# Kernel tuning notes

Measured on AMD Instinct MI355X. Metric: run time of the kernel, lower is better.

## Reference

```python
import jax, jax.numpy as jnp
import numpy as np

B, S, D = 2, 2048, 2048
H, KVH, DH = 16, 4, 128
WIN = 128
THETA = 10000.0  # local rope (layer_idx=0 -> local/sliding path)


def setup_inputs() -> dict:
    key = jax.random.key(0)
    ks = jax.random.split(key, 5)
    return {
        "x": jax.random.normal(ks[0], (B, S, D), dtype=jnp.float32),
        "Wq": jax.random.normal(ks[1], (H * DH, D), dtype=jnp.float32) * 0.02,
        "Wk": jax.random.normal(ks[2], (KVH * DH, D), dtype=jnp.float32) * 0.02,
        "Wv": jax.random.normal(ks[3], (KVH * DH, D), dtype=jnp.float32) * 0.02,
        "Wo": jax.random.normal(ks[4], (D, H * DH), dtype=jnp.float32) * 0.02,
    }


def _rotate_half(t):
    half = t.shape[-1] // 2
    return jnp.concatenate([-t[..., half:], t[..., :half]], axis=-1)


def _rope_tables(seq_len, head_dim, theta, dtype):
    inv_freq = 1.0 / (theta ** (jnp.arange(0, head_dim, 2, dtype=jnp.float32) / head_dim))
    freqs = jnp.arange(seq_len, dtype=jnp.float32)[:, None] * inv_freq[None, :]  # [S, DH/2]
    # source does repeat_interleave(cos, 2, dim=-1): [S, DH]
    cos = jnp.repeat(jnp.cos(freqs), 2, axis=-1).astype(dtype)
    sin = jnp.repeat(jnp.sin(freqs), 2, axis=-1).astype(dtype)
    return cos[None, :, None, :], sin[None, :, None, :]  # broadcast over [B,S,H,DH]


def reference(x, Wq, Wk, Wv, Wo):
    b, s, _ = x.shape
    q = (x @ Wq.T).reshape(b, s, H, DH)
    k = (x @ Wk.T).reshape(b, s, KVH, DH)
    v = (x @ Wv.T).reshape(b, s, KVH, DH)

    cos, sin = _rope_tables(s, DH, THETA, x.dtype)
    q = q * cos + _rotate_half(q) * sin
    k = k * cos + _rotate_half(k) * sin

    # GQA: repeat_interleave kv heads to n_heads
    groups = H // KVH
    k = jnp.repeat(k, groups, axis=2)
    v = jnp.repeat(v, groups, axis=2)

    q = q.transpose(0, 2, 1, 3)  # [B,H,S,DH]
    k = k.transpose(0, 2, 1, 3)
    v = v.transpose(0, 2, 1, 3)

    scale = DH ** -0.5
    scores = jnp.einsum('bhqd,bhkd->bhqk', q, k) * scale  # [B,H,S,S]

    # faithful local mask from source: q_idx >= k_idx - window_size
    iq = jnp.arange(s)[:, None]
    ik = jnp.arange(s)[None, :]
    mask = iq >= (ik - WIN)  # [S,S]
    scores = jnp.where(mask[None, None, :, :], scores, jnp.float32(-jnp.inf).astype(scores.dtype))

    attn = jax.nn.softmax(scores, axis=-1)
    out = jnp.einsum('bhqk,bhkd->bhqd', attn, v)
    out = out.transpose(0, 2, 1, 3).reshape(b, s, H * DH)
    return out @ Wo.T
```

## Files before the change

### kernel.cpp

```cpp
#include <hip/hip_runtime.h>
#include <hip/hip_bf16.h>

using bf16 = __hip_bfloat16;
typedef __attribute__((ext_vector_type(8))) short short8;
typedef __attribute__((ext_vector_type(4))) float floatx4;

#define AS1 __attribute__((address_space(1)))
#define AS3 __attribute__((address_space(3)))

__device__ __forceinline__ floatx4 mfma16(short8 a, short8 b, floatx4 c) {
  return __builtin_amdgcn_mfma_f32_16x16x32_bf16(a, b, c, 0, 0, 0);
}
__device__ __forceinline__ void gload16(const bf16* g, bf16* l) {
  __builtin_amdgcn_global_load_lds((const AS1 unsigned*)g, (AS3 unsigned*)l, 16, 0, 0);
}

__global__ void cast_all_k(const float* __restrict__ x, const float* __restrict__ Wq,
                           const float* __restrict__ Wk, const float* __restrict__ Wv,
                           const float* __restrict__ Wo, bf16* __restrict__ xb,
                           bf16* __restrict__ wqkv, bf16* __restrict__ wo_b) {
  int blk = blockIdx.x;
  const float* src;
  bf16* dst;
  int off;
  if (blk < 8192)       { src = x;  dst = xb;                 off = blk; }
  else if (blk < 12288) { src = Wq; dst = wqkv;               off = blk - 8192; }
  else if (blk < 13312) { src = Wk; dst = wqkv + 2048 * 2048; off = blk - 12288; }
  else if (blk < 14336) { src = Wv; dst = wqkv + 2560 * 2048; off = blk - 13312; }
  else                  { src = Wo; dst = wo_b;               off = blk - 14336; }
  int i = (off * 256 + threadIdx.x) * 4;
  float4 v = *(const float4*)(src + i);
  bf16 t[4] = {__float2bfloat16(v.x), __float2bfloat16(v.y),
               __float2bfloat16(v.z), __float2bfloat16(v.w)};
  *(ushort4*)(dst + i) = *(const ushort4*)t;
}

template <typename OutT>
__global__ __launch_bounds__(256, 2)
void gemm_bt(const bf16* __restrict__ A, const bf16* __restrict__ B,
             OutT* __restrict__ C, int M, int N, int K) {
  __shared__ alignas(16) bf16 As[128 * 32];
  __shared__ alignas(16) bf16 Bs[128 * 32];
  const int tid = threadIdx.x;
  const int w = tid >> 6, lane = tid & 63, l16 = lane & 15, quad = lane >> 4;
  const int bm = blockIdx.x << 7, bn = blockIdx.y << 7;
  const int wm = (w & 1) << 6, wn = (w >> 1) << 6;

  const int r = tid >> 2, p = tid & 3;
  const int g0 = (p ^ ((r >> 1) & 3)) << 3;
  const int g1 = (p ^ (((r + 64) >> 1) & 3)) << 3;
  const bf16* Ag0 = A + (long)(bm + r) * K + g0;
  const bf16* Ag1 = A + (long)(bm + r + 64) * K + g1;
  const bf16* Bg0 = B + (long)(bn + r) * K + g0;
  const bf16* Bg1 = B + (long)(bn + r + 64) * K + g1;
  bf16* Asw = As + (w << 9);
  bf16* Bsw = Bs + (w << 9);

  floatx4 acc[4][4];
#pragma unroll
  for (int i = 0; i < 4; ++i)
#pragma unroll
    for (int j = 0; j < 4; ++j) acc[i][j] = (floatx4)(0.0f);

  for (int k0 = 0; k0 < K; k0 += 32) {
    gload16(Ag0 + k0, Asw);
    gload16(Ag1 + k0, Asw + 2048);
    gload16(Bg0 + k0, Bsw);
    gload16(Bg1 + k0, Bsw + 2048);
    __syncthreads();
    short8 af[4], bfv[4];
#pragma unroll
    for (int mi = 0; mi < 4; ++mi) {
      int row = wm + (mi << 4) + l16;
      int pos = quad ^ ((row >> 1) & 3);
      af[mi] = *(const short8*)(As + row * 32 + pos * 8);
    }
#pragma unroll
    for (int ni = 0; ni < 4; ++ni) {
      int row = wn + (ni << 4) + l16;
      int pos = quad ^ ((row >> 1) & 3);
      bfv[ni] = *(const short8*)(Bs + row * 32 + pos * 8);
    }
#pragma unroll
    for (int mi = 0; mi < 4; ++mi)
#pragma unroll
      for (int ni = 0; ni < 4; ++ni)
        acc[mi][ni] = mfma16(af[mi], bfv[ni], acc[mi][ni]);
    __syncthreads();
  }

#pragma unroll
  for (int mi = 0; mi < 4; ++mi)
#pragma unroll
    for (int ni = 0; ni < 4; ++ni)
#pragma unroll
      for (int rr = 0; rr < 4; ++rr) {
        int row = bm + wm + (mi << 4) + (quad << 2) + rr;
        int col = bn + wn + (ni << 4) + l16;
        float v = acc[mi][ni][rr];
        if constexpr (sizeof(OutT) == 2)
          C[(long)row * N + col] = __float2bfloat16(v);
        else
          C[(long)row * N + col] = v;
      }
}

__global__ void rope_k(const bf16* __restrict__ qkv, bf16* __restrict__ Q,
                       bf16* __restrict__ Kd) {
  int idx = blockIdx.x * 256 + threadIdx.x;
  int d = idx & 63;
  int rest = idx >> 6;
  int head = rest % 20;
  int token = rest / 20;
  int s = token & 2047;
  int b = token >> 11;
  const float C0 = 0.20762050593046439f;
  float i1 = (float)(d >> 1);
  float inv1 = exp2f(-i1 * C0);
  float inv2 = exp2f(-(i1 + 32.0f) * C0);
  float a1 = (float)s * inv1, a2 = (float)s * inv2;
  float s1, c1, s2, c2;
  sincosf(a1, &s1, &c1);
  sincosf(a2, &s2, &c2);
  if (head < 16) {
    const bf16* p = qkv + (long)token * 3072 + head * 128 + d;
    float xlo = __bfloat162float(p[0]), xhi = __bfloat162float(p[64]);
    const float sc = 0.08838834764831845f * 1.4426950408889634f;
    float olo = (xlo * c1 - xhi * s1) * sc;
    float ohi = (xhi * c2 + xlo * s2) * sc;
    bf16* q = Q + ((long)((b << 4) + head) * 2048 + s) * 128 + d;
    q[0] = __float2bfloat16(olo);
    q[64] = __float2bfloat16(ohi);
  } else {
    int kvh = head - 16;
    const bf16* p = qkv + (long)token * 3072 + 2048 + kvh * 128 + d;
    float xlo = __bfloat162float(p[0]), xhi = __bfloat162float(p[64]);
    float olo = xlo * c1 - xhi * s1;
    float ohi = xhi * c2 + xlo * s2;
    bf16* kk = Kd + ((long)((b << 2) + kvh) * 2048 + s) * 128 + d;
    kk[0] = __float2bfloat16(olo);
    kk[64] = __float2bfloat16(ohi);
  }
}

__global__ void vtrans_k(const bf16* __restrict__ qkv, bf16* __restrict__ Vt) {
  __shared__ bf16 t[32][33];
  int x = threadIdx.x, y = threadIdx.y;
  int s0 = blockIdx.x << 5, d0 = blockIdx.y << 5, bkv = blockIdx.z;
  int b = bkv >> 2, kvh = bkv & 3;
  const bf16* src = qkv + (long)((b << 11) + s0) * 3072 + 2560 + kvh * 128 + d0;
#pragma unroll
  for (int yy = y; yy < 32; yy += 8) t[yy][x] = src[(long)yy * 3072 + x];
  __syncthreads();
  bf16* dst = Vt + (long)((bkv << 7) + d0) * 2048 + s0;
#pragma unroll
  for (int yy = y; yy < 32; yy += 8) dst[(long)yy * 2048 + x] = t[x][yy];
}

__global__ __launch_bounds__(256, 2)
void attn_k(const bf16* __restrict__ Q, const bf16* __restrict__ K,
            const bf16* __restrict__ V, bf16* __restrict__ O) {
  __shared__ alignas(16) bf16 lk[128 * 128];
  __shared__ alignas(16) bf16 lv[128 * 128];
  __shared__ alignas(16) bf16 lpA[4 * 16 * 64];
  __shared__ alignas(16) bf16 lpB[4 * 16 * 64];
  const int tid = threadIdx.x, w = tid >> 6, lane = tid & 63;
  const int l16 = lane & 15, quad = lane >> 4;
  const int bx = blockIdx.x;
  const int qa0 = bx << 6, qb0 = (31 - bx) << 6;
  const int nkA = (bx >> 1) + 2;
  int nkBt = ((31 - bx) >> 1) + 2;
  const int nkB = nkBt < 16 ? nkBt : 16;
  const int jmA = (bx >> 1) + 1, jmB = ((31 - bx) >> 1) + 1;
  const int bh = blockIdx.y, b = bh >> 4, h = bh & 15, kvh = h >> 2;
  const bf16* Qp = Q + (long)bh * 2048 * 128;
  const bf16* Kp = K + (long)((b << 2) + kvh) * 2048 * 128;
  const bf16* Vp = V + (long)((b << 2) + kvh) * 128 * 2048;

  short8 qfA[4], qfB[4];
#pragma unroll
  for (int kc = 0; kc < 4; ++kc) {
    qfA[kc] = *(const short8*)(Qp + (long)(qa0 + (w << 4) + l16) * 128 + kc * 32 + quad * 8);
    qfB[kc] = *(const short8*)(Qp + (long)(qb0 + (w << 4) + l16) * 128 + kc * 32 + quad * 8);
  }

  floatx4 oA[8], oB[8];
#pragma unroll
  for (int i = 0; i < 8; ++i) { oA[i] = (floatx4)(0.0f); oB[i] = (floatx4)(0.0f); }
  float lA = 0.0f, lB = 0.0f;

  bf16* pwA = lpA + (w << 10);
  bf16* pwB = lpB + (w << 10);
  const int sw = l16 & 7;

  auto tile = [&](auto bothc, int k0, bool maskA, bool maskB) {
    constexpr bool BOTH = decltype(bothc)::value;
    floatx4 sA[8], sB[8];
#pragma unroll
    for (int kt = 0; kt < 8; ++kt) {
      sB[kt] = (floatx4)(0.0f);
      if constexpr (BOTH) sA[kt] = (floatx4)(0.0f);
    }
#pragma unroll
    for (int kc = 0; kc < 4; ++kc) {
#pragma unroll
      for (int kt = 0; kt < 8; ++kt) {
        int row = (kt << 4) + l16;
        int g = (kc << 2) + quad;
        int pos = (g & 8) | ((g & 7) ^ (row & 7));
        short8 kf = *(const short8*)(lk + row * 128 + pos * 8);
        sB[kt] = mfma16(kf, qfB[kc], sB[kt]);
        if constexpr (BOTH) sA[kt] = mfma16(kf, qfA[kc], sA[kt]);
      }
    }
    if (maskB) {
      int qg = qb0 + (w << 4) + l16 + 128;
#pragma unroll
      for (int kt = 0; kt < 8; ++kt)
#pragma unroll
        for (int rr = 0; rr < 4; ++rr) {
          int kg = k0 + (kt << 4) + (quad << 2) + rr;
          if (kg > qg) sB[kt][rr] = -1e30f;
        }
    }
    if constexpr (BOTH) {
      if (maskA) {
        int qg = qa0 + (w << 4) + l16 + 128;
#pragma unroll
        for (int kt = 0; kt < 8; ++kt)
#pragma unroll
          for (int rr = 0; rr < 4; ++rr) {
            int kg = k0 + (kt << 4) + (quad << 2) + rr;
            if (kg > qg) sA[kt][rr] = -1e30f;
          }
      }
    }
#pragma unroll
    for (int hh = 0; hh < 2; ++hh) {
#pragma unroll
      for (int t = 0; t < 4; ++t) {
        int kt = (hh << 2) + t;
        int slot = (t << 2) + quad;
        int sl = ((((slot >> 1) ^ sw) << 1) | (quad & 1)) << 2;
        {
          float p0 = exp2f(sB[kt][0]), p1 = exp2f(sB[kt][1]);
          float p2 = exp2f(sB[kt][2]), p3 = exp2f(sB[kt][3]);
          lB += (p0 + p1) + (p2 + p3);
          bf16 tb[4] = {__float2bfloat16(p0), __float2bfloat16(p1),
                        __float2bfloat16(p2), __float2bfloat16(p3)};
          *(ushort4*)(pwB + (l16 << 6) + sl) = *(const ushort4*)tb;
        }
        if constexpr (BOTH) {
          float p0 = exp2f(sA[kt][0]), p1 = exp2f(sA[kt][1]);
          float p2 = exp2f(sA[kt][2]), p3 = exp2f(sA[kt][3]);
          lA += (p0 + p1) + (p2 + p3);
          bf16 ta[4] = {__float2bfloat16(p0), __float2bfloat16(p1),
                        __float2bfloat16(p2), __float2bfloat16(p3)};
          *(ushort4*)(pwA + (l16 << 6) + sl) = *(const ushort4*)ta;
        }
      }
#pragma unroll
      for (int kcl = 0; kcl < 2; ++kcl) {
        int pp = ((kcl << 2) + quad) ^ sw;
        short8 pfB = *(const short8*)(pwB + (l16 << 6) + (pp << 3));
        short8 pfA;
        if constexpr (BOTH) pfA = *(const short8*)(pwA + (l16 << 6) + (pp << 3));
        int kcg = (hh << 1) + kcl;
#pragma unroll
        for (int nd = 0; nd < 8; ++nd) {
          int vrow = (nd << 4) + l16;
          int g = (kcg << 2) + quad;
          int pos = (g & 8) | ((g & 7) ^ (vrow & 7));
          short8 vf = *(const short8*)(lv + vrow * 128 + pos * 8);
          oB[nd] = mfma16(pfB, vf, oB[nd]);
          if constexpr (BOTH) oA[nd] = mfma16(pfA, vf, oA[nd]);
        }
      }
    }
  };

  for (int j = 0; j < nkB; ++j) {
    const int k0 = j << 7;
#pragma unroll
    for (int i = 0; i < 8; ++i) {
      int c = i * 256 + tid;
      int row = c >> 4, pos = c & 15;
      int g = (pos & 8) | ((pos & 7) ^ (row & 7));
      gload16(Kp + (long)(k0 + row) * 128 + g * 8, lk + (i * 256 + (w << 6)) * 8);
    }
#pragma unroll
    for (int i = 0; i < 8; ++i) {
      int c = i * 256 + tid;
      int row = c >> 4, pos = c & 15;
      int g = (pos & 8) | ((pos & 7) ^ (row & 7));
      gload16(Vp + (long)row * 2048 + k0 + g * 8, lv + (i * 256 + (w << 6)) * 8);
    }
    __syncthreads();
    if (j < nkA)
      tile(std::integral_constant<bool, true>{}, k0, j == jmA, j == jmB);
    else
      tile(std::integral_constant<bool, false>{}, k0, false, j == jmB);
    __syncthreads();
  }

  lA += __shfl_xor(lA, 16, 64); lA += __shfl_xor(lA, 32, 64);
  lB += __shfl_xor(lB, 16, 64); lB += __shfl_xor(lB, 32, 64);
  float liA = 1.0f / lA, liB = 1.0f / lB;
  float rlA[4], rlB[4];
#pragma unroll
  for (int rr = 0; rr < 4; ++rr) {
    int src = (quad << 2) + rr;
    rlA[rr] = __shfl(liA, src, 64);
    rlB[rr] = __shfl(liB, src, 64);
  }

  bf16* OpA = O + ((long)(b << 11) + qa0 + (w << 4)) * 2048 + (h << 7);
  bf16* OpB = O + ((long)(b << 11) + qb0 + (w << 4)) * 2048 + (h << 7);
#pragma unroll
  for (int nd = 0; nd < 8; ++nd)
#pragma unroll
    for (int rr = 0; rr < 4; ++rr) {
      int row = (quad << 2) + rr;
      int col = (nd << 4) + l16;
      OpA[(long)row * 2048 + col] = __float2bfloat16(oA[nd][rr] * rlA[rr]);
      OpB[(long)row * 2048 + col] = __float2bfloat16(oB[nd][rr] * rlB[rr]);
    }
}

extern "C" void kernel_launch(void* const* d_in, const int* in_sizes, int n_in,
                              void* d_out, int out_size, void* d_ws, size_t ws_size,
                              hipStream_t stream) {
  (void)in_sizes; (void)n_in; (void)out_size; (void)ws_size;
  const float* x  = (const float*)d_in[0];
  const float* Wq = (const float*)d_in[1];
  const float* Wk = (const float*)d_in[2];
  const float* Wv = (const float*)d_in[3];
  const float* Wo = (const float*)d_in[4];
  char* ws = (char*)d_ws;
  bf16* xb   = (bf16*)(ws);
  bf16* wqkv = (bf16*)(ws + 16777216);
  bf16* wo_b = (bf16*)(ws + 29360128);
  bf16* qkv  = (bf16*)(ws + 37748736);
  bf16* Qr   = (bf16*)(ws + 62914560);
  bf16* Kr   = (bf16*)(ws + 79691776);
  bf16* Vt   = (bf16*)(ws + 83886080);
  bf16* Ob   = xb;
  float* out = (float*)d_out;

  cast_all_k<<<18432, 256, 0, stream>>>(x, Wq, Wk, Wv, Wo, xb, wqkv, wo_b);

  gemm_bt<bf16><<<dim3(32, 24), 256, 0, stream>>>(xb, wqkv, qkv, 4096, 3072, 2048);
  rope_k<<<20480, 256, 0, stream>>>(qkv, Qr, Kr);
  vtrans_k<<<dim3(64, 4, 8), dim3(32, 8), 0, stream>>>(qkv, Vt);
  attn_k<<<dim3(16, 32), 256, 0, stream>>>(Qr, Kr, Vt, Ob);
  gemm_bt<float><<<dim3(32, 16), 256, 0, stream>>>(Ob, wo_b, out, 4096, 2048, 2048);
}
```

Baseline: 311.3 us.

## Double-buffer 64-key K/V tiles in attention and use fast sincos in rope

The attention kernel now uses 64-key tiles instead of 128 and keeps two LDS buffers for K and V. The next tile's global-to-LDS loads are issued before the current tile is computed, so load latency can overlap with MFMA work. Tile counts, the mask tile indices and the V swizzle are rewritten for the smaller tile, and the extra loop iterations add per-tile overhead. The rope kernel also switches to the fast __sincosf intrinsic, trading accuracy at large angles for speed.

```diff
diff --git a/kernel.cpp b/kernel.cpp
--- a/kernel.cpp
+++ b/kernel.cpp
@@ -120,8 +120,8 @@
   float inv2 = exp2f(-(i1 + 32.0f) * C0);
   float a1 = (float)s * inv1, a2 = (float)s * inv2;
   float s1, c1, s2, c2;
-  sincosf(a1, &s1, &c1);
-  sincosf(a2, &s2, &c2);
+  __sincosf(a1, &s1, &c1);
+  __sincosf(a2, &s2, &c2);
   if (head < 16) {
     const bf16* p = qkv + (long)token * 3072 + head * 128 + d;
     float xlo = __bfloat162float(p[0]), xhi = __bfloat162float(p[64]);
@@ -160,18 +160,18 @@
 __global__ __launch_bounds__(256, 2)
 void attn_k(const bf16* __restrict__ Q, const bf16* __restrict__ K,
             const bf16* __restrict__ V, bf16* __restrict__ O) {
-  __shared__ alignas(16) bf16 lk[128 * 128];
-  __shared__ alignas(16) bf16 lv[128 * 128];
+  __shared__ alignas(16) bf16 lk[2][64 * 128];
+  __shared__ alignas(16) bf16 lv[2][128 * 64];
   __shared__ alignas(16) bf16 lpA[4 * 16 * 64];
   __shared__ alignas(16) bf16 lpB[4 * 16 * 64];
   const int tid = threadIdx.x, w = tid >> 6, lane = tid & 63;
   const int l16 = lane & 15, quad = lane >> 4;
   const int bx = blockIdx.x;
   const int qa0 = bx << 6, qb0 = (31 - bx) << 6;
-  const int nkA = (bx >> 1) + 2;
-  int nkBt = ((31 - bx) >> 1) + 2;
-  const int nkB = nkBt < 16 ? nkBt : 16;
-  const int jmA = (bx >> 1) + 1, jmB = ((31 - bx) >> 1) + 1;
+  const int nkA = bx + 3;
+  int nkBt = 34 - bx;
+  const int nkB = nkBt < 32 ? nkBt : 32;
+  const int jmA = bx + 2, jmB = 33 - bx;
   const int bh = blockIdx.y, b = bh >> 4, h = bh & 15, kvh = h >> 2;
   const bf16* Qp = Q + (long)bh * 2048 * 128;
   const bf16* Kp = K + (long)((b << 2) + kvh) * 2048 * 128;
@@ -193,22 +193,43 @@
   bf16* pwB = lpB + (w << 10);
   const int sw = l16 & 7;
 
-  auto tile = [&](auto bothc, int k0, bool maskA, bool maskB) {
+  auto stage = [&](int j, int bufi) {
+    const int k0 = j << 6;
+    bf16* lkb = &lk[bufi][0];
+    bf16* lvb = &lv[bufi][0];
+#pragma unroll
+    for (int i = 0; i < 4; ++i) {
+      int c = i * 256 + tid;
+      int row = c >> 4, pos = c & 15;
+      int grp = (pos & 8) | ((pos & 7) ^ (row & 7));
+      gload16(Kp + (long)(k0 + row) * 128 + grp * 8, lkb + (i * 256 + (w << 6)) * 8);
+    }
+#pragma unroll
+    for (int i = 0; i < 4; ++i) {
+      int c = i * 256 + tid;
+      int row = c >> 3, grp = (c & 7) ^ (row & 7);
+      gload16(Vp + (long)row * 2048 + k0 + grp * 8, lvb + (i * 256 + (w << 6)) * 8);
+    }
+  };
+
+  auto tile = [&](auto bothc, int k0, bool maskA, bool maskB, int bufi) {
     constexpr bool BOTH = decltype(bothc)::value;
-    floatx4 sA[8], sB[8];
-#pragma unroll
-    for (int kt = 0; kt < 8; ++kt) {
+    const bf16* lkb = &lk[bufi][0];
+    const bf16* lvb = &lv[bufi][0];
+    floatx4 sA[4], sB[4];
+#pragma unroll
+    for (int kt = 0; kt < 4; ++kt) {
       sB[kt] = (floatx4)(0.0f);
       if constexpr (BOTH) sA[kt] = (floatx4)(0.0f);
     }
 #pragma unroll
     for (int kc = 0; kc < 4; ++kc) {
 #pragma unroll
-      for (int kt = 0; kt < 8; ++kt) {
+      for (int kt = 0; kt < 4; ++kt) {
         int row = (kt << 4) + l16;
         int g = (kc << 2) + quad;
         int pos = (g & 8) | ((g & 7) ^ (row & 7));
-        short8 kf = *(const short8*)(lk + row * 128 + pos * 8);
+        short8 kf = *(const short8*)(lkb + row * 128 + pos * 8);
         sB[kt] = mfma16(kf, qfB[kc], sB[kt]);
         if constexpr (BOTH) sA[kt] = mfma16(kf, qfA[kc], sA[kt]);
       }
@@ -216,7 +237,7 @@
     if (maskB) {
       int qg = qb0 + (w << 4) + l16 + 128;
 #pragma unroll
-      for (int kt = 0; kt < 8; ++kt)
+      for (int kt = 0; kt < 4; ++kt)
 #pragma unroll
         for (int rr = 0; rr < 4; ++rr) {
           int kg = k0 + (kt << 4) + (quad << 2) + rr;
@@ -227,7 +248,7 @@
       if (maskA) {
         int qg = qa0 + (w << 4) + l16 + 128;
 #pragma unroll
-        for (int kt = 0; kt < 8; ++kt)
+        for (int kt = 0; kt < 4; ++kt)
 #pragma unroll
           for (int rr = 0; rr < 4; ++rr) {
             int kg = k0 + (kt << 4) + (quad << 2) + rr;
@@ -236,70 +257,53 @@
       }
     }
 #pragma unroll
-    for (int hh = 0; hh < 2; ++hh) {
-#pragma unroll
-      for (int t = 0; t < 4; ++t) {
-        int kt = (hh << 2) + t;
-        int slot = (t << 2) + quad;
-        int sl = ((((slot >> 1) ^ sw) << 1) | (quad & 1)) << 2;
-        {
-          float p0 = exp2f(sB[kt][0]), p1 = exp2f(sB[kt][1]);
-          float p2 = exp2f(sB[kt][2]), p3 = exp2f(sB[kt][3]);
-          lB += (p0 + p1) + (p2 + p3);
-          bf16 tb[4] = {__float2bfloat16(p0), __float2bfloat16(p1),
-                        __float2bfloat16(p2), __float2bfloat16(p3)};
-          *(ushort4*)(pwB + (l16 << 6) + sl) = *(const ushort4*)tb;
-        }
-        if constexpr (BOTH) {
-          float p0 = exp2f(sA[kt][0]), p1 = exp2f(sA[kt][1]);
-          float p2 = exp2f(sA[kt][2]), p3 = exp2f(sA[kt][3]);
-          lA += (p0 + p1) + (p2 + p3);
-          bf16 ta[4] = {__float2bfloat16(p0), __float2bfloat16(p1),
-                        __float2bfloat16(p2), __float2bfloat16(p3)};
-          *(ushort4*)(pwA + (l16 << 6) + sl) = *(const ushort4*)ta;
-        }
-      }
-#pragma unroll
-      for (int kcl = 0; kcl < 2; ++kcl) {
-        int pp = ((kcl << 2) + quad) ^ sw;
-        short8 pfB = *(const short8*)(pwB + (l16 << 6) + (pp << 3));
-        short8 pfA;
-        if constexpr (BOTH) pfA = *(const short8*)(pwA + (l16 << 6) + (pp << 3));
-        int kcg = (hh << 1) + kcl;
-#pragma unroll
-        for (int nd = 0; nd < 8; ++nd) {
-          int vrow = (nd << 4) + l16;
-          int g = (kcg << 2) + quad;
-          int pos = (g & 8) | ((g & 7) ^ (vrow & 7));
-          short8 vf = *(const short8*)(lv + vrow * 128 + pos * 8);
-          oB[nd] = mfma16(pfB, vf, oB[nd]);
-          if constexpr (BOTH) oA[nd] = mfma16(pfA, vf, oA[nd]);
-        }
+    for (int t = 0; t < 4; ++t) {
+      int slot = (t << 2) + quad;
+      int sl = ((((slot >> 1) ^ sw) << 1) | (quad & 1)) << 2;
+      {
+        float p0 = exp2f(sB[t][0]), p1 = exp2f(sB[t][1]);
+        float p2 = exp2f(sB[t][2]), p3 = exp2f(sB[t][3]);
+        lB += (p0 + p1) + (p2 + p3);
+        bf16 tb[4] = {__float2bfloat16(p0), __float2bfloat16(p1),
+                      __float2bfloat16(p2), __float2bfloat16(p3)};
+        *(ushort4*)(pwB + (l16 << 6) + sl) = *(const ushort4*)tb;
+      }
+      if constexpr (BOTH) {
+        float p0 = exp2f(sA[t][0]), p1 = exp2f(sA[t][1]);
+        float p2 = exp2f(sA[t][2]), p3 = exp2f(sA[t][3]);
+        lA += (p0 + p1) + (p2 + p3);
+        bf16 ta[4] = {__float2bfloat16(p0), __float2bfloat16(p1),
+                      __float2bfloat16(p2), __float2bfloat16(p3)};
+        *(ushort4*)(pwA + (l16 << 6) + sl) = *(const ushort4*)ta;
+      }
+    }
+#pragma unroll
+    for (int kcl = 0; kcl < 2; ++kcl) {
+      int pp = ((kcl << 2) + quad) ^ sw;
+      short8 pfB = *(const short8*)(pwB + (l16 << 6) + (pp << 3));
+      short8 pfA;
+      if constexpr (BOTH) pfA = *(const short8*)(pwA + (l16 << 6) + (pp << 3));
+      int g = (kcl << 2) + quad;
+#pragma unroll
+      for (int nd = 0; nd < 8; ++nd) {
+        int vrow = (nd << 4) + l16;
+        int vpos = g ^ (vrow & 7);
+        short8 vf = *(const short8*)(lvb + vrow * 64 + (vpos << 3));
+        oB[nd] = mfma16(pfB, vf, oB[nd]);
+        if constexpr (BOTH) oA[nd] = mfma16(pfA, vf, oA[nd]);
       }
     }
   };
 
+  stage(0, 0);
+  __syncthreads();
   for (int j = 0; j < nkB; ++j) {
-    const int k0 = j << 7;
-#pragma unroll
-    for (int i = 0; i < 8; ++i) {
-      int c = i * 256 + tid;
-      int row = c >> 4, pos = c & 15;
-      int g = (pos & 8) | ((pos & 7) ^ (row & 7));
-      gload16(Kp + (long)(k0 + row) * 128 + g * 8, lk + (i * 256 + (w << 6)) * 8);
-    }
-#pragma unroll
-    for (int i = 0; i < 8; ++i) {
-      int c = i * 256 + tid;
-      int row = c >> 4, pos = c & 15;
-      int g = (pos & 8) | ((pos & 7) ^ (row & 7));
-      gload16(Vp + (long)row * 2048 + k0 + g * 8, lv + (i * 256 + (w << 6)) * 8);
-    }
-    __syncthreads();
+    if (j + 1 < nkB) stage(j + 1, (j + 1) & 1);
+    const int k0 = j << 6;
     if (j < nkA)
-      tile(std::integral_constant<bool, true>{}, k0, j == jmA, j == jmB);
+      tile(std::integral_constant<bool, true>{}, k0, j == jmA, j == jmB, j & 1);
     else
-      tile(std::integral_constant<bool, false>{}, k0, false, j == jmB);
+      tile(std::integral_constant<bool, false>{}, k0, false, j == jmB, j & 1);
     __syncthreads();
   }
 
```

After: 294.7 us. -5.3%, faster.
